# Kernel tuning notes

Hardware: AMD Instinct MI355X
Metric: run time of the kernel (lower is better)

The kernel has to match this reference:

```python
import jax, jax.numpy as jnp
import numpy as np

SIG = 0.5  # radial Gaussian width of basis profiles

def _profiles(ksize, radii):
    c = (ksize - 1) // 2
    ys, xs = np.mgrid[-c:c + 1, -c:c + 1].astype(np.float32)
    rr = np.sqrt(ys ** 2 + xs ** 2)
    phi = np.arctan2(ys, xs)
    f = np.exp(-((rr[None] - np.asarray(radii, np.float32)[:, None, None]) ** 2) / (2 * SIG ** 2))
    f = f / f.sum(axis=(1, 2), keepdims=True)
    return f.astype(np.float32), phi.astype(np.float32)

def _steerable_basis():
    # create_radial(2) -> 5x5 kernels; k=0 uses radii {0,1,2}, k>=1 uses radii {1,2}
    f0, _ = _profiles(5, [0.0, 1.0, 2.0])          # [3,5,5]
    f, phi = _profiles(5, [1.0, 2.0])              # [2,5,5]
    Bc = np.stack([f * np.cos(k * phi) for k in (1, 2)])  # [2,2,5,5]
    Bs = np.stack([f * np.sin(k * phi) for k in (1, 2)])  # [2,2,5,5]
    return jnp.asarray(f0), jnp.asarray(Bc), jnp.asarray(Bs)

def _ortho_basis():
    # OrthoKernelBase.create_radial(3) -> 7x7 (cos phi, sin phi) vector kernels, radii {1,2,3}
    f, phi = _profiles(7, [1.0, 2.0, 3.0])
    return jnp.asarray(f * np.cos(phi)), jnp.asarray(f * np.sin(phi))

def _convT(x, k, stride=2):
    # torch conv_transpose2d(stride=2, padding='same') -> output H*stride
    return jax.lax.conv_transpose(x, k, strides=(stride, stride), padding='SAME',
                                  dimension_numbers=('NCHW', 'OIHW', 'NCHW'))

def setup_inputs() -> dict:
    key = jax.random.key(0)
    ks = jax.random.split(key, 6)
    B, Cin, Cout, H, W = 8, 64, 64, 64, 64
    x = jax.random.normal(ks[0], (B, Cin, H, W), jnp.float32)
    s = np.float32(1.0 / np.sqrt(Cin * 25))
    w0 = jax.random.normal(ks[1], (Cout, Cin, 3), jnp.float32) * s
    wc = jax.random.normal(ks[2], (2, Cout, Cin, 2), jnp.float32) * s
    ws = jax.random.normal(ks[3], (2, Cout, Cin, 2), jnp.float32) * s
    wa = jax.random.normal(ks[4], (Cout, Cin, 3), jnp.float32) * np.float32(1.0 / np.sqrt(Cin * 49))
    b = np.float32(1.0 / np.sqrt(Cout))
    bias = jax.random.uniform(ks[5], (Cout,), jnp.float32, minval=-b, maxval=b)
    return {"x": x, "w0": w0, "wc": wc, "ws": ws, "wa": wa, "bias": bias}

def reference(x, w0, wc, ws, wa, bias):
    B0, Bc, Bs = _steerable_basis()
    Ac, As = _ortho_basis()
    n_out = w0.shape[0]
    # --- attention: ortho conv-transpose producing a steering vector field (u,v)
    #     per output feature at the output resolution ---
    Ka = jnp.concatenate([jnp.einsum('oir,rhw->oihw', wa, Ac),
                          jnp.einsum('oir,rhw->oihw', wa, As)], axis=0)  # [2*n_out,n_in,7,7]
    uv = _convT(x, Ka)                      # [B, 2*n_out, 2H, 2W]
    u, v = uv[:, :n_out], uv[:, n_out:]
    # --- normalize_vector + tanh(rho) ---
    rho_raw = jnp.sqrt(u * u + v * v + 1e-8)
    un, vn = u / rho_raw, v / rho_raw        # unit steering vector (cos t, sin t)
    rho = jnp.tanh(rho_raw)
    c1, s1 = un, vn
    c2, s2 = un * un - vn * vn, 2.0 * un * vn   # Chebyshev: cos 2t, sin 2t
    # --- synthesize steerable kernels from basis and run one stacked conv-transpose ---
    K0 = jnp.einsum('oir,rhw->oihw', w0, B0)
    Kc = jnp.einsum('koir,krhw->koihw', wc, Bc)
    Ks = jnp.einsum('koir,krhw->koihw', ws, Bs)
    Kall = jnp.concatenate([K0, Kc[0], Ks[0], Kc[1], Ks[1]], axis=0)  # [5*n_out,n_in,5,5]
    y = _convT(x, Kall)                      # [B, 5*n_out, 2H, 2W]
    b_, _, Ho, Wo = y.shape
    y = y.reshape(b_, 5, n_out, Ho, Wo)
    out = y[:, 0] + rho * (c1 * y[:, 1] + s1 * y[:, 2] + c2 * y[:, 3] + s2 * y[:, 4])
    return out + bias[None, :, None, None]
```

## Files before the change

### kernel.cpp

```cpp
#include <hip/hip_runtime.h>
#include <math.h>


namespace {

typedef float f4 __attribute__((ext_vector_type(4)));
typedef short s8 __attribute__((ext_vector_type(8)));

constexpr int NKA = 401408;
constexpr int NKB = 512000;

__device__ __forceinline__ unsigned short f2bf(float f) {
    unsigned int u = __float_as_uint(f);
    u += 0x7fffu + ((u >> 16) & 1u);
    return (unsigned short)(u >> 16);
}

template <int PY, int PX>
constexpr unsigned bmaskA() {
    constexpr int NXA = 4 - PX, NYA = 4 - PY, NXB = 2 + PX, NYB = 2 + PY;
    unsigned m = 0;
    for (int t = 0; t < NYA * NXA; ++t) {
        int tyi = t / NXA, txi = t % NXA;
        int ty = tyi - (1 - PY), tx = txi - (1 - PX);
        if (ty >= 0 && ty < NYB && tx >= 0 && tx < NXB) m |= 1u << t;
    }
    return m;
}

__device__ void prep_body(
    const float* __restrict__ w0, const float* __restrict__ wc,
    const float* __restrict__ wsn, const float* __restrict__ wa,
    unsigned short* __restrict__ KA, unsigned short* __restrict__ KB,
    const float* SA, const float* S5)
{
    const int idx = blockIdx.x * 256 + threadIdx.x;
    if (idx < NKA) {
        int i = idx & 63;
        int e = idx >> 6;
        int oc = e & 63; e >>= 6;
        int uv = e & 1;  e >>= 1;
        int par = (e < 16) ? 0 : (e < 28) ? 1 : (e < 40) ? 2 : 3;
        int t = e - ((par == 0) ? 0 : (par == 1) ? 16 : (par == 2) ? 28 : 40);
        int py = par >> 1, px = par & 1;
        int nx = 4 - px;
        int tyi = t / nx, txi = t % nx;
        float dy = (float)(2 * tyi + py - 3), dx = (float)(2 * txi + px - 3);
        float rr = sqrtf(dy * dy + dx * dx);
        float phi = atan2f(dy, dx);
        const float* wr = wa + (oc * 64 + i) * 3;
        float v = 0.f;
#pragma unroll
        for (int r = 0; r < 3; ++r) { float d = rr - (float)(r + 1); v += wr[r] * (expf(-2.f * d * d) / SA[r]); }
        float tr = uv ? sinf(phi) : cosf(phi);
        KA[idx] = f2bf(v * tr);
    } else if (idx < NKA + NKB) {
        int j = idx - NKA;
        int i = j & 63;
        int rest = j >> 6;
        int oc = rest % 320;
        int e = rest / 320;
        int par = (e < 4) ? 0 : (e < 10) ? 1 : (e < 16) ? 2 : 3;
        int t = e - ((par == 0) ? 0 : (par == 1) ? 4 : (par == 2) ? 10 : 16);
        int py = par >> 1, px = par & 1;
        int nx = 2 + px;
        int tyi = t / nx, txi = t % nx;
        float dy = (float)(2 * tyi - 1 - py), dx = (float)(2 * txi - 1 - px);
        float rr = sqrtf(dy * dy + dx * dx);
        float phi = atan2f(dy, dx);
        int g = oc >> 6, o = oc & 63;
        float v = 0.f;
        if (g == 0) {
            const float* wr = w0 + (o * 64 + i) * 3;
#pragma unroll
            for (int r = 0; r < 3; ++r) { float d = rr - (float)r; v += wr[r] * (expf(-2.f * d * d) / S5[r]); }
        } else {
            int k = (g - 1) >> 1, sn = (g - 1) & 1;
            const float* wsel = ((sn == 0) ? wc : wsn) + ((k * 64 + o) * 64 + i) * 2;
            float s = 0.f;
#pragma unroll
            for (int r = 0; r < 2; ++r) { float d = rr - (float)(r + 1); s += wsel[r] * (expf(-2.f * d * d) / S5[r + 1]); }
            float ang = (float)(k + 1) * phi;
            v = s * ((sn == 0) ? cosf(ang) : sinf(ang));
        }
        KB[j] = f2bf(v);
    }
}

__device__ void transpose_body(
    const float* __restrict__ x, unsigned short* __restrict__ Xt, float* LFraw)
{
    float (*LF)[65] = (float (*)[65])LFraw;
    const int t = threadIdx.x;
    const int j = blockIdx.x - 3568;
    const int iyp = j % 68, b = j / 68;
    const int iy = iyp - 2;
    unsigned int* Xtu = (unsigned int*)(Xt + (size_t)(b * 68 + iyp) * 68 * 64);
    if (iy < 0 || iy >= 64) {
        for (int k = t; k < 68 * 32; k += 256) Xtu[k] = 0u;
        return;
    }
    const float* xb = x + (size_t)b * 262144 + iy * 64;
#pragma unroll
    for (int it = 0; it < 16; ++it) {
        int ch = it * 4 + (t >> 6);
        LF[ch][t & 63] = xb[(size_t)ch * 4096 + (t & 63)];
    }
    __syncthreads();
    if (t < 128) {
        int colidx = t >> 5;
        int ixp = (colidx < 2) ? colidx : 64 + colidx;
        Xtu[ixp * 32 + (t & 31)] = 0u;
    }
    const int lane = t & 63, w = t >> 6;
#pragma unroll
    for (int k = 0; k < 8; ++k) {
        int it = w * 8 + k;
        int ix = 2 * it + (lane >> 5);
        int ch = 2 * (lane & 31);
        unsigned int pack = (unsigned int)f2bf(LF[ch][ix]) | ((unsigned int)f2bf(LF[ch + 1][ix]) << 16);
        const int ixp = ix + 2;
        const int gslot = ((lane & 31) >> 2) ^ (ixp & 7);
        Xtu[ixp * 32 + gslot * 4 + ((lane & 31) & 3)] = pack;
    }
}

__global__ __launch_bounds__(256) void setup_kernel(
    const float* __restrict__ w0, const float* __restrict__ wc,
    const float* __restrict__ wsn, const float* __restrict__ wa,
    const float* __restrict__ x,
    unsigned short* __restrict__ KA, unsigned short* __restrict__ KB,
    unsigned short* __restrict__ Xt,
    float sa0, float sa1, float sa2, float s50, float s51, float s52)
{
    __shared__ float LFraw[64 * 65];
    const float SA[3] = {sa0, sa1, sa2};
    const float S5[3] = {s50, s51, s52};
    if (blockIdx.x < 3568) prep_body(w0, wc, wsn, wa, KA, KB, SA, S5);
    else                   transpose_body(x, Xt, LFraw);
}

template <int PY, int PX>
__device__ __forceinline__ void mfma_loop(
    const unsigned short* __restrict__ Xs,
    const unsigned short* __restrict__ KA, const unsigned short* __restrict__ KB,
    const float* __restrict__ bias, float* __restrict__ out,
    int b, int oy, int obase, int lr, int hi)
{
    constexpr int NXA = 4 - PX, NYA = 4 - PY, NTA = NYA * NXA;
    constexpr int PAR = 2 * PY + PX;
    constexpr int TBA = (PAR == 0) ? 0 : (PAR == 1) ? 16 : (PAR == 2) ? 28 : 40;
    constexpr int TBB = (PAR == 0) ? 0 : (PAR == 1) ? 4  : (PAR == 2) ? 10 : 16;
    constexpr unsigned BM = bmaskA<PY, PX>();

    const unsigned short* ka = KA + TBA * 8192  + (obase + lr) * 64 + hi * 8;
    const unsigned short* kb = KB + TBB * 20480 + (obase + lr) * 64 + hi * 8;

    f4 accA[2][4];
    f4 accB[5][4];
#pragma unroll
    for (int uv = 0; uv < 2; ++uv)
#pragma unroll
        for (int ni = 0; ni < 4; ++ni) accA[uv][ni] = f4{0.f, 0.f, 0.f, 0.f};
#pragma unroll
    for (int g = 0; g < 5; ++g)
#pragma unroll
        for (int ni = 0; ni < 4; ++ni) accB[g][ni] = f4{0.f, 0.f, 0.f, 0.f};

    s8 a0[2], a1[2], g0[5], g1[5], x0[4], x1[4];

    auto loadA = [&](s8 (&d)[2], int t, int ks) {
#pragma unroll
        for (int uv = 0; uv < 2; ++uv)
            d[uv] = *(const s8*)(ka + t * 8192 + uv * 4096 + ks * 32);
    };
    auto loadG = [&](s8 (&d)[5], int tB, int ks) {
#pragma unroll
        for (int g = 0; g < 5; ++g)
            d[g] = *(const s8*)(kb + tB * 20480 + g * 4096 + ks * 32);
    };
    auto loadX = [&](s8 (&d)[4], int tyi, int txi, int ks) {
#pragma unroll
        for (int ni = 0; ni < 4; ++ni) {
            const int rx = ni * 16 + lr + txi + PX;
            const int gz = (ks * 4 + hi) ^ (rx & 7);
            d[ni] = *(const s8*)(Xs + ((tyi * 68 + rx) * 8 + gz) * 8);
        }
    };
    auto mmA = [&](s8 (&a)[2], s8 (&xx)[4]) {
#pragma unroll
        for (int uv = 0; uv < 2; ++uv)
#pragma unroll
            for (int ni = 0; ni < 4; ++ni)
                accA[uv][ni] = __builtin_amdgcn_mfma_f32_16x16x32_bf16(a[uv], xx[ni], accA[uv][ni], 0, 0, 0);
    };
    auto mmB = [&](s8 (&gg)[5], s8 (&xx)[4]) {
#pragma unroll
        for (int g = 0; g < 5; ++g)
#pragma unroll
            for (int ni = 0; ni < 4; ++ni)
                accB[g][ni] = __builtin_amdgcn_mfma_f32_16x16x32_bf16(gg[g], xx[ni], accB[g][ni], 0, 0, 0);
    };

    loadA(a0, 0, 0);
    loadX(x0, 0, 0, 0);
    if (BM & 1u) loadG(g0, 0, 0);

    int tyi = 0, txi = 0, tB = 0;
#pragma unroll
    for (int t = 0; t < NTA; ++t) {
        const bool bv = (BM >> t) & 1u;
        loadA(a1, t, 1);
        loadX(x1, tyi, txi, 1);
        if (bv) loadG(g1, tB, 1);
        mmA(a0, x0);
        if (bv) mmB(g0, x0);
        const int txn = (txi + 1 == NXA) ? 0 : txi + 1;
        const int tyn = (txi + 1 == NXA) ? tyi + 1 : tyi;
        if (t + 1 < NTA) {
            loadA(a0, t + 1, 0);
            loadX(x0, tyn, txn, 0);
            if ((BM >> (t + 1)) & 1u) loadG(g0, tB + (bv ? 1 : 0), 0);
        }
        mmA(a1, x1);
        if (bv) { mmB(g1, x1); ++tB; }
        tyi = tyn; txi = txn;
    }

    const int yy = 2 * oy + PY;
#pragma unroll
    for (int ni = 0; ni < 4; ++ni) {
        const int px = ni * 16 + lr;
        const int xx = 2 * px + PX;
#pragma unroll
        for (int r2 = 0; r2 < 4; ++r2) {
            const int o = obase + hi * 4 + r2;
            const float u = accA[0][ni][r2], v = accA[1][ni][r2];
            const float rho_raw = sqrtf(u * u + v * v + 1e-8f);
            const float un = u / rho_raw, vn = v / rho_raw;
            const float rho = tanhf(rho_raw);
            const float c2 = (un - vn) * (un + vn);
            const float sp = 2.f * un * vn;
            out[((b * 64 + o) * 128 + yy) * 128 + xx] =
                accB[0][ni][r2]
                + rho * (un * accB[1][ni][r2] + vn * accB[2][ni][r2]
                       + c2 * accB[3][ni][r2] + sp * accB[4][ni][r2])
                + bias[o];
        }
    }
}

template <int PY>
__device__ __forceinline__ void fused_body(
    const unsigned short* __restrict__ Xt,
    const unsigned short* __restrict__ KA, const unsigned short* __restrict__ KB,
    const float* __restrict__ bias, float* __restrict__ out,
    int oh, unsigned short* Xs)
{
    constexpr int NYA = 4 - PY;
    const int tid = threadIdx.x;
    const int oy = blockIdx.x, b = blockIdx.y;

    {
        const int iy0p = oy + PY;
        const int lane = tid & 63;
        const unsigned short* src = Xt + ((size_t)b * 68 + iy0p) * 68 * 64;
        constexpr int NCH = (NYA * 68 * 8 + 63) / 64;
        const int wv = tid >> 6;
        for (int c = wv; c < NCH; c += 4)
            __builtin_amdgcn_global_load_lds((const unsigned int*)(src + c * 512 + lane * 8),
                                             (unsigned int*)(Xs + c * 512), 16, 0, 0);
    }
    __syncthreads();

    const int lane = tid & 63, lr = lane & 15, hi = lane >> 4;
    const int w = tid >> 6;
    const int p = w & 1, mq = w >> 1;
    const int obase = oh * 32 + mq * 16;

    if (p == 0)
        mfma_loop<PY, 0>(Xs, KA, KB, bias, out, b, oy, obase, lr, hi);
    else
        mfma_loop<PY, 1>(Xs, KA, KB, bias, out, b, oy, obase, lr, hi);
}

__global__ __launch_bounds__(256, 2) void fused_kernel(
    const unsigned short* __restrict__ Xt,
    const unsigned short* __restrict__ KA, const unsigned short* __restrict__ KB,
    const float* __restrict__ bias, float* __restrict__ out)
{
    __shared__ __align__(16) unsigned short Xs[4 * 68 * 64];
    const int z = blockIdx.z;
    const int oh = z >> 1;
    if (z & 1) fused_body<1>(Xt, KA, KB, bias, out, oh, Xs);
    else       fused_body<0>(Xt, KA, KB, bias, out, oh, Xs);
}

}

extern "C" void kernel_launch(void* const* d_in, const int* in_sizes, int n_in,
                              void* d_out, int out_size, void* d_ws, size_t ws_size,
                              hipStream_t stream)
{
    const float* x    = (const float*)d_in[0];
    const float* w0   = (const float*)d_in[1];
    const float* wc   = (const float*)d_in[2];
    const float* wsn  = (const float*)d_in[3];
    const float* wa   = (const float*)d_in[4];
    const float* bias = (const float*)d_in[5];
    float* out = (float*)d_out;

    char* wsb = (char*)d_ws;
    unsigned short* KA = (unsigned short*)(wsb);
    unsigned short* KB = (unsigned short*)(wsb + 802816);
    unsigned short* Xt = (unsigned short*)(wsb + 2097152);

    float SA[3] = {0.f, 0.f, 0.f}, S5[3] = {0.f, 0.f, 0.f};
    for (int ky = 0; ky < 7; ++ky)
        for (int kx = 0; kx < 7; ++kx) {
            float dy = (float)(ky - 3), dx = (float)(kx - 3);
            float rr = sqrtf(dy * dy + dx * dx);
            for (int r = 0; r < 3; ++r) { float d = rr - (float)(r + 1); SA[r] += expf(-2.f * d * d); }
        }
    for (int ky = 0; ky < 5; ++ky)
        for (int kx = 0; kx < 5; ++kx) {
            float dy = (float)(ky - 2), dx = (float)(kx - 2);
            float rr = sqrtf(dy * dy + dx * dx);
            for (int r = 0; r < 3; ++r) { float d = rr - (float)r; S5[r] += expf(-2.f * d * d); }
        }

    setup_kernel<<<dim3(3568 + 544), dim3(256), 0, stream>>>(
        w0, wc, wsn, wa, x, KA, KB, Xt,
        SA[0], SA[1], SA[2], S5[0], S5[1], S5[2]);

    fused_kernel<<<dim3(64, 8, 4), dim3(256), 0, stream>>>(Xt, KA, KB, bias, out);
}
```

Measured before the change: 238.1 us.

## Compute two output rows per block to reuse weight fragments across rows

Each block now handles two adjacent output rows. It loads one extra input row into LDS and doubles the per-wave accumulator tiles (8 N-fragments instead of 4), so every weight fragment loaded from global memory feeds twice as many MFMAs. The double-buffered pipeline is restructured to prefetch only weights, with input fragments read from LDS per step. In exchange, the accumulator register footprint roughly doubles (launch bounds drop to 1 block per SIMD-occupancy hint), the grid halves, and occupancy and latency hiding are reduced.

New measurement: 234.0 us. About the same (-1.7%).

```diff
diff --git a/kernel.cpp b/kernel.cpp
--- a/kernel.cpp
+++ b/kernel.cpp
@@ -145,7 +145,7 @@
     const unsigned short* __restrict__ Xs,
     const unsigned short* __restrict__ KA, const unsigned short* __restrict__ KB,
     const float* __restrict__ bias, float* __restrict__ out,
-    int b, int oy, int obase, int lr, int hi)
+    int b, int oy0, int obase, int lr, int hi)
 {
     constexpr int NXA = 4 - PX, NYA = 4 - PY, NTA = NYA * NXA;
     constexpr int PAR = 2 * PY + PX;
@@ -156,81 +156,73 @@
     const unsigned short* ka = KA + TBA * 8192  + (obase + lr) * 64 + hi * 8;
     const unsigned short* kb = KB + TBB * 20480 + (obase + lr) * 64 + hi * 8;
 
-    f4 accA[2][4];
-    f4 accB[5][4];
+    f4 accA[2][8];
+    f4 accB[5][8];
 #pragma unroll
     for (int uv = 0; uv < 2; ++uv)
 #pragma unroll
-        for (int ni = 0; ni < 4; ++ni) accA[uv][ni] = f4{0.f, 0.f, 0.f, 0.f};
+        for (int ni = 0; ni < 8; ++ni) accA[uv][ni] = f4{0.f, 0.f, 0.f, 0.f};
 #pragma unroll
     for (int g = 0; g < 5; ++g)
 #pragma unroll
-        for (int ni = 0; ni < 4; ++ni) accB[g][ni] = f4{0.f, 0.f, 0.f, 0.f};
-
-    s8 a0[2], a1[2], g0[5], g1[5], x0[4], x1[4];
-
-    auto loadA = [&](s8 (&d)[2], int t, int ks) {
+        for (int ni = 0; ni < 8; ++ni) accB[g][ni] = f4{0.f, 0.f, 0.f, 0.f};
+
+    s8 aw[2][2], gw[2][5];
+
+    {
 #pragma unroll
         for (int uv = 0; uv < 2; ++uv)
-            d[uv] = *(const s8*)(ka + t * 8192 + uv * 4096 + ks * 32);
-    };
-    auto loadG = [&](s8 (&d)[5], int tB, int ks) {
-#pragma unroll
-        for (int g = 0; g < 5; ++g)
-            d[g] = *(const s8*)(kb + tB * 20480 + g * 4096 + ks * 32);
-    };
-    auto loadX = [&](s8 (&d)[4], int tyi, int txi, int ks) {
-#pragma unroll
-        for (int ni = 0; ni < 4; ++ni) {
-            const int rx = ni * 16 + lr + txi + PX;
+            aw[0][uv] = *(const s8*)(ka + 0 * 8192 + uv * 4096 + 0 * 32);
+        if (BM & 1u) {
+#pragma unroll
+            for (int g = 0; g < 5; ++g)
+                gw[0][g] = *(const s8*)(kb + 0 * 20480 + g * 4096 + 0 * 32);
+        }
+    }
+
+#pragma unroll
+    for (int s = 0; s < 2 * NTA; ++s) {
+        const int t = s >> 1, ks = s & 1, ph = s & 1;
+        const int tyi = t / NXA, txi = t % NXA;
+        const bool bv = (BM >> t) & 1u;
+        if (s + 1 < 2 * NTA) {
+            const int tn = (s + 1) >> 1, ksn = (s + 1) & 1;
+            const int tBn = __builtin_popcount(BM & ((1u << tn) - 1u));
+#pragma unroll
+            for (int uv = 0; uv < 2; ++uv)
+                aw[ph ^ 1][uv] = *(const s8*)(ka + tn * 8192 + uv * 4096 + ksn * 32);
+            if ((BM >> tn) & 1u) {
+#pragma unroll
+                for (int g = 0; g < 5; ++g)
+                    gw[ph ^ 1][g] = *(const s8*)(kb + tBn * 20480 + g * 4096 + ksn * 32);
+            }
+        }
+        s8 xf[8];
+#pragma unroll
+        for (int ni = 0; ni < 8; ++ni) {
+            const int row = tyi + (ni >> 2);
+            const int rx = (ni & 3) * 16 + lr + txi + PX;
             const int gz = (ks * 4 + hi) ^ (rx & 7);
-            d[ni] = *(const s8*)(Xs + ((tyi * 68 + rx) * 8 + gz) * 8);
-        }
-    };
-    auto mmA = [&](s8 (&a)[2], s8 (&xx)[4]) {
+            xf[ni] = *(const s8*)(Xs + ((row * 68 + rx) * 8 + gz) * 8);
+        }
 #pragma unroll
         for (int uv = 0; uv < 2; ++uv)
 #pragma unroll
-            for (int ni = 0; ni < 4; ++ni)
-                accA[uv][ni] = __builtin_amdgcn_mfma_f32_16x16x32_bf16(a[uv], xx[ni], accA[uv][ni], 0, 0, 0);
-    };
-    auto mmB = [&](s8 (&gg)[5], s8 (&xx)[4]) {
-#pragma unroll
-        for (int g = 0; g < 5; ++g)
-#pragma unroll
-            for (int ni = 0; ni < 4; ++ni)
-                accB[g][ni] = __builtin_amdgcn_mfma_f32_16x16x32_bf16(gg[g], xx[ni], accB[g][ni], 0, 0, 0);
-    };
-
-    loadA(a0, 0, 0);
-    loadX(x0, 0, 0, 0);
-    if (BM & 1u) loadG(g0, 0, 0);
-
-    int tyi = 0, txi = 0, tB = 0;
-#pragma unroll
-    for (int t = 0; t < NTA; ++t) {
-        const bool bv = (BM >> t) & 1u;
-        loadA(a1, t, 1);
-        loadX(x1, tyi, txi, 1);
-        if (bv) loadG(g1, tB, 1);
-        mmA(a0, x0);
-        if (bv) mmB(g0, x0);
-        const int txn = (txi + 1 == NXA) ? 0 : txi + 1;
-        const int tyn = (txi + 1 == NXA) ? tyi + 1 : tyi;
-        if (t + 1 < NTA) {
-            loadA(a0, t + 1, 0);
-            loadX(x0, tyn, txn, 0);
-            if ((BM >> (t + 1)) & 1u) loadG(g0, tB + (bv ? 1 : 0), 0);
-        }
-        mmA(a1, x1);
-        if (bv) { mmB(g1, x1); ++tB; }
-        tyi = tyn; txi = txn;
-    }
-
-    const int yy = 2 * oy + PY;
-#pragma unroll
-    for (int ni = 0; ni < 4; ++ni) {
-        const int px = ni * 16 + lr;
+            for (int ni = 0; ni < 8; ++ni)
+                accA[uv][ni] = __builtin_amdgcn_mfma_f32_16x16x32_bf16(aw[ph][uv], xf[ni], accA[uv][ni], 0, 0, 0);
+        if (bv) {
+#pragma unroll
+            for (int g = 0; g < 5; ++g)
+#pragma unroll
+                for (int ni = 0; ni < 8; ++ni)
+                    accB[g][ni] = __builtin_amdgcn_mfma_f32_16x16x32_bf16(gw[ph][g], xf[ni], accB[g][ni], 0, 0, 0);
+        }
+    }
+
+#pragma unroll
+    for (int ni = 0; ni < 8; ++ni) {
+        const int yy = 2 * (oy0 + (ni >> 2)) + PY;
+        const int px = (ni & 3) * 16 + lr;
         const int xx = 2 * px + PX;
 #pragma unroll
         for (int r2 = 0; r2 < 4; ++r2) {
@@ -259,13 +251,13 @@
 {
     constexpr int NYA = 4 - PY;
     const int tid = threadIdx.x;
-    const int oy = blockIdx.x, b = blockIdx.y;
+    const int oy0 = 2 * blockIdx.x, b = blockIdx.y;
 
     {
-        const int iy0p = oy + PY;
+        const int iy0p = oy0 + PY;
         const int lane = tid & 63;
         const unsigned short* src = Xt + ((size_t)b * 68 + iy0p) * 68 * 64;
-        constexpr int NCH = (NYA * 68 * 8 + 63) / 64;
+        constexpr int NCH = ((NYA + 1) * 68 * 8 + 63) / 64;
         const int wv = tid >> 6;
         for (int c = wv; c < NCH; c += 4)
             __builtin_amdgcn_global_load_lds((const unsigned int*)(src + c * 512 + lane * 8),
@@ -279,17 +271,17 @@
     const int obase = oh * 32 + mq * 16;
 
     if (p == 0)
-        mfma_loop<PY, 0>(Xs, KA, KB, bias, out, b, oy, obase, lr, hi);
+        mfma_loop<PY, 0>(Xs, KA, KB, bias, out, b, oy0, obase, lr, hi);
     else
-        mfma_loop<PY, 1>(Xs, KA, KB, bias, out, b, oy, obase, lr, hi);
-}
-
-__global__ __launch_bounds__(256, 2) void fused_kernel(
+        mfma_loop<PY, 1>(Xs, KA, KB, bias, out, b, oy0, obase, lr, hi);
+}
+
+__global__ __launch_bounds__(256, 1) void fused_kernel(
     const unsigned short* __restrict__ Xt,
     const unsigned short* __restrict__ KA, const unsigned short* __restrict__ KB,
     const float* __restrict__ bias, float* __restrict__ out)
 {
-    __shared__ __align__(16) unsigned short Xs[4 * 68 * 64];
+    __shared__ __align__(16) unsigned short Xs[22016];
     const int z = blockIdx.z;
     const int oh = z >> 1;
     if (z & 1) fused_body<1>(Xt, KA, KB, bias, out, oh, Xs);
@@ -333,5 +325,5 @@
         w0, wc, wsn, wa, x, KA, KB, Xt,
         SA[0], SA[1], SA[2], S5[0], S5[1], S5[2]);
 
-    fused_kernel<<<dim3(64, 8, 4), dim3(256), 0, stream>>>(Xt, KA, KB, bias, out);
-}
+    fused_kernel<<<dim3(32, 8, 4), dim3(256), 0, stream>>>(Xt, KA, KB, bias, out);
+}
```

## Stage steerable weights in LDS per parity/out-channel block and loop over row groups

Applied to the files above, without the earlier changes.

Reorganizes the fused conv-transpose kernel so each block handles one output parity and one 16-channel slice. The steerable basis weights (KB) are re-laid out with a swizzle and loaded once into LDS, then reused across 8 groups of 4 output rows each. Attention weights are preloaded into registers per k-half. Each wave now works on its own output row, not a parity. This cuts repeated global weight loads but drops occupancy to one 144KB-LDS block per CU with only 256 blocks. The X loads and compute are also serialized per row group, with no overlap.

Result: faster. 201.1 us (-15.5%).

```diff
diff --git a/kernel.cpp b/kernel.cpp
--- a/kernel.cpp
+++ b/kernel.cpp
@@ -9,6 +9,7 @@
 
 constexpr int NKA = 401408;
 constexpr int NKB = 512000;
+constexpr int OFFBC[4] = {0, 81920, 204800, 327680};
 
 __device__ __forceinline__ unsigned short f2bf(float f) {
     unsigned int u = __float_as_uint(f);
@@ -56,19 +57,25 @@
         KA[idx] = f2bf(v * tr);
     } else if (idx < NKA + NKB) {
         int j = idx - NKA;
-        int i = j & 63;
-        int rest = j >> 6;
-        int oc = rest % 320;
-        int e = rest / 320;
-        int par = (e < 4) ? 0 : (e < 10) ? 1 : (e < 16) ? 2 : 3;
-        int t = e - ((par == 0) ? 0 : (par == 1) ? 4 : (par == 2) ? 10 : 16);
+        int par = (j < OFFBC[1]) ? 0 : (j < OFFBC[2]) ? 1 : (j < OFFBC[3]) ? 2 : 3;
         int py = par >> 1, px = par & 1;
         int nx = 2 + px;
+        int ntb = (2 + py) * nx;
+        int j2 = j - OFFBC[par];
+        int per = ntb * 5120;
+        int mq = j2 / per;
+        int r1 = j2 - mq * per;
+        int t = r1 / 5120;
+        int r2 = r1 - t * 5120;
+        int g = r2 >> 10;
+        int oc16 = (r2 >> 6) & 15;
+        int i_s = r2 & 63;
+        int i = (((i_s >> 3) ^ (oc16 & 7)) << 3) | (i_s & 7);
+        int o = mq * 16 + oc16;
         int tyi = t / nx, txi = t % nx;
         float dy = (float)(2 * tyi - 1 - py), dx = (float)(2 * txi - 1 - px);
         float rr = sqrtf(dy * dy + dx * dx);
         float phi = atan2f(dy, dx);
-        int g = oc >> 6, o = oc & 63;
         float v = 0.f;
         if (g == 0) {
             const float* wr = w0 + (o * 64 + i) * 3;
@@ -141,159 +148,148 @@
 }
 
 template <int PY, int PX>
-__device__ __forceinline__ void mfma_loop(
-    const unsigned short* __restrict__ Xs,
+__device__ __forceinline__ void conv_body(
+    const unsigned short* __restrict__ Xt,
     const unsigned short* __restrict__ KA, const unsigned short* __restrict__ KB,
     const float* __restrict__ bias, float* __restrict__ out,
-    int b, int oy, int obase, int lr, int hi)
+    int mq, int tg, char* lds)
 {
     constexpr int NXA = 4 - PX, NYA = 4 - PY, NTA = NYA * NXA;
+    constexpr int NXB = 2 + PX, NYB = 2 + PY, NTB = NYB * NXB;
     constexpr int PAR = 2 * PY + PX;
     constexpr int TBA = (PAR == 0) ? 0 : (PAR == 1) ? 16 : (PAR == 2) ? 28 : 40;
-    constexpr int TBB = (PAR == 0) ? 0 : (PAR == 1) ? 4  : (PAR == 2) ? 10 : 16;
     constexpr unsigned BM = bmaskA<PY, PX>();
-
-    const unsigned short* ka = KA + TBA * 8192  + (obase + lr) * 64 + hi * 8;
-    const unsigned short* kb = KB + TBB * 20480 + (obase + lr) * 64 + hi * 8;
-
-    f4 accA[2][4];
-    f4 accB[5][4];
-#pragma unroll
-    for (int uv = 0; uv < 2; ++uv)
-#pragma unroll
-        for (int ni = 0; ni < 4; ++ni) accA[uv][ni] = f4{0.f, 0.f, 0.f, 0.f};
-#pragma unroll
-    for (int g = 0; g < 5; ++g)
-#pragma unroll
-        for (int ni = 0; ni < 4; ++ni) accB[g][ni] = f4{0.f, 0.f, 0.f, 0.f};
-
-    s8 a0[2], a1[2], g0[5], g1[5], x0[4], x1[4];
-
-    auto loadA = [&](s8 (&d)[2], int t, int ks) {
-#pragma unroll
-        for (int uv = 0; uv < 2; ++uv)
-            d[uv] = *(const s8*)(ka + t * 8192 + uv * 4096 + ks * 32);
-    };
-    auto loadG = [&](s8 (&d)[5], int tB, int ks) {
-#pragma unroll
-        for (int g = 0; g < 5; ++g)
-            d[g] = *(const s8*)(kb + tB * 20480 + g * 4096 + ks * 32);
-    };
+    constexpr int XROWS = NYA + 3;
+    constexpr int XCH = (XROWS * 8704 + 1023) / 1024;
+    constexpr int WBCH = NTB * 10;
+
+    unsigned short* WB = (unsigned short*)lds;
+    unsigned short* Xs = (unsigned short*)(lds + WBCH * 1024);
+
+    const int tid = threadIdx.x;
+    const int lane = tid & 63, lr = lane & 15, hi = lane >> 4;
+    const int wv = tid >> 6;
+    const int obase = mq * 16;
+
+    {
+        const unsigned short* kbsrc = KB + OFFBC[PAR] + mq * (NTB * 5120);
+        for (int c = wv; c < WBCH; c += 4)
+            __builtin_amdgcn_global_load_lds((const unsigned int*)(kbsrc + c * 512 + lane * 8),
+                                             (unsigned int*)(WB + c * 512), 16, 0, 0);
+    }
+
     auto loadX = [&](s8 (&d)[4], int tyi, int txi, int ks) {
+        const int lrow = wv + tyi;
 #pragma unroll
         for (int ni = 0; ni < 4; ++ni) {
             const int rx = ni * 16 + lr + txi + PX;
             const int gz = (ks * 4 + hi) ^ (rx & 7);
-            d[ni] = *(const s8*)(Xs + ((tyi * 68 + rx) * 8 + gz) * 8);
+            d[ni] = *(const s8*)(Xs + ((lrow * 68 + rx) * 8 + gz) * 8);
         }
     };
-    auto mmA = [&](s8 (&a)[2], s8 (&xx)[4]) {
+
+    for (int gi = 0; gi < 8; ++gi) {
+        const int G = tg * 8 + gi;
+        const int b = G >> 4;
+        const int oy0 = (G & 15) * 4;
+
+        {
+            const unsigned short* xsrc = Xt + (size_t)(b * 68 + oy0 + PY) * 4352;
+            for (int c = wv; c < XCH; c += 4)
+                __builtin_amdgcn_global_load_lds((const unsigned int*)(xsrc + c * 512 + lane * 8),
+                                                 (unsigned int*)(Xs + c * 512), 16, 0, 0);
+        }
+        __syncthreads();
+
+        f4 accA[2][4];
+        f4 accB[5][4];
 #pragma unroll
         for (int uv = 0; uv < 2; ++uv)
 #pragma unroll
-            for (int ni = 0; ni < 4; ++ni)
-                accA[uv][ni] = __builtin_amdgcn_mfma_f32_16x16x32_bf16(a[uv], xx[ni], accA[uv][ni], 0, 0, 0);
-    };
-    auto mmB = [&](s8 (&gg)[5], s8 (&xx)[4]) {
+            for (int ni = 0; ni < 4; ++ni) accA[uv][ni] = f4{0.f, 0.f, 0.f, 0.f};
 #pragma unroll
         for (int g = 0; g < 5; ++g)
 #pragma unroll
-            for (int ni = 0; ni < 4; ++ni)
-                accB[g][ni] = __builtin_amdgcn_mfma_f32_16x16x32_bf16(gg[g], xx[ni], accB[g][ni], 0, 0, 0);
-    };
-
-    loadA(a0, 0, 0);
-    loadX(x0, 0, 0, 0);
-    if (BM & 1u) loadG(g0, 0, 0);
-
-    int tyi = 0, txi = 0, tB = 0;
-#pragma unroll
-    for (int t = 0; t < NTA; ++t) {
-        const bool bv = (BM >> t) & 1u;
-        loadA(a1, t, 1);
-        loadX(x1, tyi, txi, 1);
-        if (bv) loadG(g1, tB, 1);
-        mmA(a0, x0);
-        if (bv) mmB(g0, x0);
-        const int txn = (txi + 1 == NXA) ? 0 : txi + 1;
-        const int tyn = (txi + 1 == NXA) ? tyi + 1 : tyi;
-        if (t + 1 < NTA) {
-            loadA(a0, t + 1, 0);
-            loadX(x0, tyn, txn, 0);
-            if ((BM >> (t + 1)) & 1u) loadG(g0, tB + (bv ? 1 : 0), 0);
-        }
-        mmA(a1, x1);
-        if (bv) { mmB(g1, x1); ++tB; }
-        tyi = tyn; txi = txn;
-    }
-
-    const int yy = 2 * oy + PY;
-#pragma unroll
-    for (int ni = 0; ni < 4; ++ni) {
-        const int px = ni * 16 + lr;
-        const int xx = 2 * px + PX;
-#pragma unroll
-        for (int r2 = 0; r2 < 4; ++r2) {
-            const int o = obase + hi * 4 + r2;
-            const float u = accA[0][ni][r2], v = accA[1][ni][r2];
-            const float rho_raw = sqrtf(u * u + v * v + 1e-8f);
-            const float un = u / rho_raw, vn = v / rho_raw;
-            const float rho = tanhf(rho_raw);
-            const float c2 = (un - vn) * (un + vn);
-            const float sp = 2.f * un * vn;
-            out[((b * 64 + o) * 128 + yy) * 128 + xx] =
-                accB[0][ni][r2]
-                + rho * (un * accB[1][ni][r2] + vn * accB[2][ni][r2]
-                       + c2 * accB[3][ni][r2] + sp * accB[4][ni][r2])
-                + bias[o];
-        }
-    }
-}
-
-template <int PY>
-__device__ __forceinline__ void fused_body(
-    const unsigned short* __restrict__ Xt,
-    const unsigned short* __restrict__ KA, const unsigned short* __restrict__ KB,
-    const float* __restrict__ bias, float* __restrict__ out,
-    int oh, unsigned short* Xs)
-{
-    constexpr int NYA = 4 - PY;
-    const int tid = threadIdx.x;
-    const int oy = blockIdx.x, b = blockIdx.y;
-
-    {
-        const int iy0p = oy + PY;
-        const int lane = tid & 63;
-        const unsigned short* src = Xt + ((size_t)b * 68 + iy0p) * 68 * 64;
-        constexpr int NCH = (NYA * 68 * 8 + 63) / 64;
-        const int wv = tid >> 6;
-        for (int c = wv; c < NCH; c += 4)
-            __builtin_amdgcn_global_load_lds((const unsigned int*)(src + c * 512 + lane * 8),
-                                             (unsigned int*)(Xs + c * 512), 16, 0, 0);
-    }
-    __syncthreads();
-
-    const int lane = tid & 63, lr = lane & 15, hi = lane >> 4;
-    const int w = tid >> 6;
-    const int p = w & 1, mq = w >> 1;
-    const int obase = oh * 32 + mq * 16;
-
-    if (p == 0)
-        mfma_loop<PY, 0>(Xs, KA, KB, bias, out, b, oy, obase, lr, hi);
-    else
-        mfma_loop<PY, 1>(Xs, KA, KB, bias, out, b, oy, obase, lr, hi);
-}
-
-__global__ __launch_bounds__(256, 2) void fused_kernel(
+            for (int ni = 0; ni < 4; ++ni) accB[g][ni] = f4{0.f, 0.f, 0.f, 0.f};
+
+#pragma unroll
+        for (int ksp = 0; ksp < 2; ++ksp) {
+            s8 aA[NTA][2];
+#pragma unroll
+            for (int t = 0; t < NTA; ++t)
+#pragma unroll
+                for (int uv = 0; uv < 2; ++uv)
+                    aA[t][uv] = *(const s8*)(KA + (((TBA + t) * 2 + uv) * 64 + obase + lr) * 64 + ksp * 32 + hi * 8);
+
+            s8 xf[2][4];
+            loadX(xf[0], 0, 0, ksp);
+#pragma unroll
+            for (int t = 0; t < NTA; ++t) {
+                const int ph = t & 1;
+                const bool bv = (BM >> t) & 1u;
+                const int tB = __builtin_popcount(BM & ((1u << t) - 1u));
+                if (t + 1 < NTA) loadX(xf[ph ^ 1], (t + 1) / NXA, (t + 1) % NXA, ksp);
+                s8 gw[5];
+                if (bv) {
+#pragma unroll
+                    for (int g = 0; g < 5; ++g)
+                        gw[g] = *(const s8*)(WB + ((tB * 5 + g) * 16 + lr) * 64 + ((ksp * 4 + hi) ^ (lr & 7)) * 8);
+                }
+#pragma unroll
+                for (int uv = 0; uv < 2; ++uv)
+#pragma unroll
+                    for (int ni = 0; ni < 4; ++ni)
+                        accA[uv][ni] = __builtin_amdgcn_mfma_f32_16x16x32_bf16(aA[t][uv], xf[ph][ni], accA[uv][ni], 0, 0, 0);
+                if (bv) {
+#pragma unroll
+                    for (int g = 0; g < 5; ++g)
+#pragma unroll
+                        for (int ni = 0; ni < 4; ++ni)
+                            accB[g][ni] = __builtin_amdgcn_mfma_f32_16x16x32_bf16(gw[g], xf[ph][ni], accB[g][ni], 0, 0, 0);
+                }
+            }
+        }
+
+        const int yy = 2 * (oy0 + wv) + PY;
+#pragma unroll
+        for (int ni = 0; ni < 4; ++ni) {
+            const int px = ni * 16 + lr;
+            const int xx = 2 * px + PX;
+#pragma unroll
+            for (int r2 = 0; r2 < 4; ++r2) {
+                const int o = obase + hi * 4 + r2;
+                const float u = accA[0][ni][r2], v = accA[1][ni][r2];
+                const float rho_raw = sqrtf(u * u + v * v + 1e-8f);
+                const float un = u / rho_raw, vn = v / rho_raw;
+                const float rho = tanhf(rho_raw);
+                const float c2 = (un - vn) * (un + vn);
+                const float sp = 2.f * un * vn;
+                out[((b * 64 + o) * 128 + yy) * 128 + xx] =
+                    accB[0][ni][r2]
+                    + rho * (un * accB[1][ni][r2] + vn * accB[2][ni][r2]
+                           + c2 * accB[3][ni][r2] + sp * accB[4][ni][r2])
+                    + bias[o];
+            }
+        }
+        __syncthreads();
+    }
+}
+
+__global__ __launch_bounds__(256, 1) void fused_kernel(
     const unsigned short* __restrict__ Xt,
     const unsigned short* __restrict__ KA, const unsigned short* __restrict__ KB,
     const float* __restrict__ bias, float* __restrict__ out)
 {
-    __shared__ __align__(16) unsigned short Xs[4 * 68 * 64];
-    const int z = blockIdx.z;
-    const int oh = z >> 1;
-    if (z & 1) fused_body<1>(Xt, KA, KB, bias, out, oh, Xs);
-    else       fused_body<0>(Xt, KA, KB, bias, out, oh, Xs);
+    __shared__ __align__(16) char lds[144384];
+    const int tg = blockIdx.x;
+    const int y = blockIdx.y;
+    const int mq = y & 3;
+    switch (y >> 2) {
+        case 0:  conv_body<0, 0>(Xt, KA, KB, bias, out, mq, tg, lds); break;
+        case 1:  conv_body<0, 1>(Xt, KA, KB, bias, out, mq, tg, lds); break;
+        case 2:  conv_body<1, 0>(Xt, KA, KB, bias, out, mq, tg, lds); break;
+        default: conv_body<1, 1>(Xt, KA, KB, bias, out, mq, tg, lds); break;
+    }
 }
 
 }
@@ -333,5 +329,5 @@
         w0, wc, wsn, wa, x, KA, KB, Xt,
         SA[0], SA[1], SA[2], S5[0], S5[1], S5[2]);
 
-    fused_kernel<<<dim3(64, 8, 4), dim3(256), 0, stream>>>(Xt, KA, KB, bias, out);
-}
+    fused_kernel<<<dim3(16, 16), dim3(256), 0, stream>>>(Xt, KA, KB, bias, out);
+}
```
